# Kernel tuning notes

Measured on AMD Instinct MI355X. Metric: run time of the kernel, lower is better.

## Reference

```python
import jax, jax.numpy as jnp
import numpy as np

GAMMA = 1.0
BANDWIDTH = 0  # 0 => no Sakoe-Chiba band
LARGE = 1e30   # stand-in for +inf; exact in the softmin limit, NaN-safe under autodiff


def _pairwise_sq_dist(x, y):
    # x:[B,N,d], y:[B,M,d] -> D:[B,N,M] squared Euclidean
    x2 = jnp.sum(x * x, axis=-1)[:, :, None]
    y2 = jnp.sum(y * y, axis=-1)[:, None, :]
    return x2 + y2 - 2.0 * jnp.einsum('bnd,bmd->bnm', x, y)


def _softdtw(D, gamma=GAMMA, bw=BANDWIDTH):
    # Anti-diagonal wavefront: scan over p = i0 + j0 in [0, N+M-2].
    # Diagonal is stored indexed by row i0; carry = (diag p-2, diag p-1).
    B, N, M = D.shape
    idx = jnp.arange(N)

    def step(carry, p):
        prev2, prev = carry                      # each [B, N]
        j0 = p - idx                             # column index per row
        valid = (j0 >= 0) & (j0 < M)
        if bw > 0:
            valid = valid & (jnp.abs(idx - j0) <= bw)
        Dg = D[:, idx, jnp.clip(j0, 0, M - 1)]   # [B, N]
        inf_col = jnp.full((B, 1), LARGE, D.dtype)
        # R[i0-1, j0-1] lives on diag p-2 at row i0-1
        r_nw = jnp.concatenate([inf_col, prev2[:, :-1]], axis=1)
        # virtual boundary R[0,0] = 0 feeds cell (i0=0, j0=0)
        r_nw = jnp.where((idx == 0) & (p == 0), jnp.zeros((), D.dtype), r_nw)
        # R[i0-1, j0] on diag p-1 at row i0-1; R[i0, j0-1] on diag p-1 at row i0
        r_n = jnp.concatenate([inf_col, prev[:, :-1]], axis=1)
        r_w = prev
        # stable softmin with gamma smoothing
        r0, r1, r2 = -r_nw / gamma, -r_n / gamma, -r_w / gamma
        rmax = jnp.maximum(jnp.maximum(r0, r1), r2)
        rsum = jnp.exp(r0 - rmax) + jnp.exp(r1 - rmax) + jnp.exp(r2 - rmax)
        softmin = -gamma * (jnp.log(rsum) + rmax)
        cur = jnp.where(valid, Dg + softmin, LARGE)
        return (prev, cur), None

    init = (jnp.full((B, N), LARGE, D.dtype), jnp.full((B, N), LARGE, D.dtype))
    (_, last), _ = jax.lax.scan(step, init, jnp.arange(N + M - 1))
    # With bw == 0 (or bw >= |N-M|), the loss is R[:, N, M] == last diag at row N-1.
    return last[:, N - 1]


def setup_inputs() -> dict:
    key = jax.random.key(0)
    k1, k2 = jax.random.split(key)
    x = jax.random.normal(k1, (128, 512, 64), dtype=jnp.float32)
    y = jax.random.normal(k2, (128, 512, 64), dtype=jnp.float32)
    return {"x": x, "y": y}


def reference(x, y):
    D = _pairwise_sq_dist(x, y)
    return _softdtw(D)
```

## Files before the change

### kernel.cpp

```cpp
#include <hip/hip_runtime.h>
#include <hip/hip_bf16.h>

#define LARGE_F 1e30f
#define LOG2E_F 1.4426950408889634f
#define LN2_F   0.6931471805599453f

constexpr int BB = 128;
constexpr int NN = 512;
constexpr int MM = 512;
constexpr int KK = 64;
constexpr int PBATCH = 262656;
constexpr size_t NEED = (size_t)BB * PBATCH * 2 + 4096;

typedef __attribute__((ext_vector_type(8))) short short8;
typedef __attribute__((ext_vector_type(4))) float f32x4;

__device__ __forceinline__ float wave_shr1(float v, float bound) {
    const int r = __builtin_amdgcn_update_dpp(__float_as_int(bound), __float_as_int(v),
                                              0x138, 0xf, 0xf, false);
    return __int_as_float(r);
}

__device__ __forceinline__ unsigned pack_bf16(float a, float b) {
    __hip_bfloat16 ha = __float2bfloat16(a);
    __hip_bfloat16 hb = __float2bfloat16(b);
    return (unsigned)*(unsigned short*)&ha | ((unsigned)*(unsigned short*)&hb << 16);
}

__device__ __forceinline__ float fast_exp2(float x) { return __builtin_amdgcn_exp2f(x); }
__device__ __forceinline__ float fast_log2(float x) { return __builtin_amdgcn_logf(x); }

__global__ __launch_bounds__(256, 2) void sdtw_dist(const float* __restrict__ x,
                                                    const float* __restrict__ y,
                                                    unsigned short* __restrict__ Dws) {
    __shared__ __align__(16) unsigned short xbf[128][88];
    __shared__ __align__(16) unsigned short ybf[128][88];
    __shared__ float x2s[128], y2s[128];
    __shared__ float xpart[128][2], ypart[128][2];
    unsigned short (*dt)[132] = (unsigned short (*)[132])(&xbf[0][0]);

    const int bid  = blockIdx.x;
    const int xcd  = bid & 7, sidx = bid >> 3;
    const int g    = sidx >> 4, tile = sidx & 15;
    const int b    = xcd + (g << 3);
    const int ti   = (tile >> 2) << 7, tj = (tile & 3) << 7;
    const int t    = threadIdx.x;

    const float* xb = x + ((size_t)b * NN + ti) * KK;
    const float* yb = y + ((size_t)b * MM + tj) * KK;

    {
        const int r = t >> 1, h = t & 1;
        const float* xr = xb + r * KK + h * 32;
        const float* yr = yb + r * KK + h * 32;
        float sx = 0.f, sy = 0.f;
        unsigned xu[16], yu[16];
#pragma unroll
        for (int q = 0; q < 8; ++q) {
            const float4 v = *(const float4*)(xr + 4 * q);
            sx = fmaf(v.x, v.x, fmaf(v.y, v.y, fmaf(v.z, v.z, fmaf(v.w, v.w, sx))));
            xu[2 * q]     = pack_bf16(v.x, v.y);
            xu[2 * q + 1] = pack_bf16(v.z, v.w);
            const float4 u = *(const float4*)(yr + 4 * q);
            sy = fmaf(u.x, u.x, fmaf(u.y, u.y, fmaf(u.z, u.z, fmaf(u.w, u.w, sy))));
            yu[2 * q]     = pack_bf16(u.x, u.y);
            yu[2 * q + 1] = pack_bf16(u.z, u.w);
        }
#pragma unroll
        for (int q = 0; q < 4; ++q) {
            *(uint4*)(&xbf[r][h * 32 + q * 8]) = make_uint4(xu[4*q], xu[4*q+1], xu[4*q+2], xu[4*q+3]);
            *(uint4*)(&ybf[r][h * 32 + q * 8]) = make_uint4(yu[4*q], yu[4*q+1], yu[4*q+2], yu[4*q+3]);
        }
        xpart[r][h] = sx; ypart[r][h] = sy;
    }
    __syncthreads();
    if (t < 128) x2s[t] = xpart[t][0] + xpart[t][1];
    else         y2s[t - 128] = ypart[t - 128][0] + ypart[t - 128][1];
    __syncthreads();

    const int w    = t >> 6, lane = t & 63;
    const int wr   = (w >> 1) << 6, wc = (w & 1) << 6;
    const int fr   = lane & 15;
    const int fk   = (lane >> 4) << 3;

    f32x4 acc[4][4] = {};
#pragma unroll
    for (int c = 0; c < 2; ++c) {
        short8 A[4], Bf[4];
#pragma unroll
        for (int a = 0; a < 4; ++a)
            A[a] = *(const short8*)(&xbf[wr + (a << 4) + fr][(c << 5) + fk]);
#pragma unroll
        for (int bb = 0; bb < 4; ++bb)
            Bf[bb] = *(const short8*)(&ybf[wc + (bb << 4) + fr][(c << 5) + fk]);
#pragma unroll
        for (int a = 0; a < 4; ++a)
#pragma unroll
            for (int bb = 0; bb < 4; ++bb)
                acc[a][bb] = __builtin_amdgcn_mfma_f32_16x16x32_bf16(
                    A[a], Bf[bb], acc[a][bb], 0, 0, 0);
    }
    __syncthreads();

    {
        const int er = (lane >> 4) << 2;
        const int ec = lane & 15;
#pragma unroll
        for (int a = 0; a < 4; ++a) {
#pragma unroll
            for (int bb = 0; bb < 4; ++bb) {
                const int lcol = wc + (bb << 4) + ec;
                const float yy = y2s[lcol];
#pragma unroll
                for (int reg = 0; reg < 4; ++reg) {
                    const int lrow = wr + (a << 4) + er + reg;
                    const float d = (x2s[lrow] + yy - 2.f * acc[a][bb][reg]) * LOG2E_F;
                    __hip_bfloat16 hh = __float2bfloat16(d);
                    dt[lrow][lcol] = *(unsigned short*)&hh;
                }
            }
        }
    }
    __syncthreads();

    {
        unsigned short* Dg = Dws + (size_t)b * PBATCH;
#pragma unroll 4
        for (int r = w; r < 128; r += 4) {
            const int gi = ti + r;
            const int base = 512 * gi + (gi + tj);
            Dg[base + lane]      = dt[r][lane];
            Dg[base + lane + 64] = dt[r][lane + 64];
        }
    }
}

__global__ __launch_bounds__(512, 1) void sdtw_dp(const unsigned short* __restrict__ Dws,
                                                  float* __restrict__ out) {
    __shared__ __align__(16) float hnd[3][8][16];
    const int b    = blockIdx.x;
    const int tid  = threadIdx.x;
    const int lane = tid & 63;
    const int wv   = tid >> 6;
    const int k0   = wv << 2;

    if (tid < 384) ((float*)hnd)[tid] = LARGE_F;
    __syncthreads();

    const char* Dbase = (const char*)Dws;
    unsigned off = (unsigned)b * 525312u + (unsigned)tid * 1024u + (unsigned)(k0 << 5);

    float cur = LARGE_F;
    float nw  = (tid == 0) ? 0.f : LARGE_F;
    float res = 0.f;
    float hband_prev = LARGE_F;
    const bool haveup = (wv > 0);
    const bool l0     = (lane == 0);

    uint4 c0 = *(const uint4*)(Dbase + off);
    uint4 c1 = *(const uint4*)(Dbase + off + 16);
    off += 32;

    int m0 = 0, m1 = 2;
#pragma unroll 1
    for (int e = 0; e < 71; ++e) {
        const int k = e - wv;
        if (k >= k0 && k < k0 + 36) {
            const unsigned q[8] = {c0.x, c0.y, c0.z, c0.w, c1.x, c1.y, c1.z, c1.w};
            float d[16];
#pragma unroll
            for (int u = 0; u < 16; ++u) {
                const unsigned w_ = q[u >> 1];
                d[u] = __uint_as_float((u & 1) ? (w_ & 0xffff0000u) : (w_ << 16));
            }
            c0 = *(const uint4*)(Dbase + off);
            c1 = *(const uint4*)(Dbase + off + 16);
            off += 32;
            __builtin_amdgcn_sched_barrier(0);

            if (k == k0 && haveup) {
                const int m2 = 3 - m0 - m1;
                hband_prev = hnd[m2][wv - 1][15];
            }
            const float hband = haveup ? hnd[m1][wv - 1][lane & 15] : LARGE_F;
            float h[16];
#pragma unroll
            for (int u = 0; u < 16; ++u) {
                const float nvec = wave_shr1(cur, LARGE_F);
                const float hu = __int_as_float(__builtin_amdgcn_readlane(
                    __float_as_int((u == 0) ? hband_prev : hband),
                    (u == 0) ? 15 : (u - 1)));
                const float n  = (haveup && l0) ? hu : nvec;
                const float mn = fminf(fminf(cur, n), nw);
                const float mx = fmaxf(fmaxf(cur, n), nw);
                const float md = __builtin_amdgcn_fmed3f(cur, n, nw);
                const float sm = mn - fast_log2(1.f + fast_exp2(mn - md) + fast_exp2(mn - mx));
                const float newc = d[u] + sm;
                h[u] = newc;
                nw = n; cur = newc;
            }
            if (k == 63) res = h[14];
            hband_prev = hband;
            if (lane == 63) {
                *(float4*)(&hnd[m0][wv][0])  = make_float4(h[0], h[1], h[2], h[3]);
                *(float4*)(&hnd[m0][wv][4])  = make_float4(h[4], h[5], h[6], h[7]);
                *(float4*)(&hnd[m0][wv][8])  = make_float4(h[8], h[9], h[10], h[11]);
                *(float4*)(&hnd[m0][wv][12]) = make_float4(h[12], h[13], h[14], h[15]);
            }
        }
        asm volatile("s_waitcnt lgkmcnt(0)" ::: "memory");
        __builtin_amdgcn_s_barrier();
        m0 = (m0 == 2) ? 0 : m0 + 1;
        m1 = (m1 == 2) ? 0 : m1 + 1;
    }
    if (tid == 511) out[b] = res * LN2_F;
}

__global__ __launch_bounds__(512) void sdtw_fused_naive(const float* __restrict__ x,
                                                        const float* __restrict__ y,
                                                        float* __restrict__ out) {
    __shared__ float rbuf[3][NN];
    __shared__ float y2s[MM];
    const int b = blockIdx.x;
    const int i = threadIdx.x;

    const float* xrow  = x + ((size_t)b * NN + i) * KK;
    const float* ybase = y + (size_t)b * MM * KK;

    float xr[KK];
    float x2 = 0.f;
#pragma unroll
    for (int k = 0; k < KK; k += 4) {
        const float4 v = *(const float4*)(xrow + k);
        xr[k] = v.x; xr[k + 1] = v.y; xr[k + 2] = v.z; xr[k + 3] = v.w;
        x2 = fmaf(v.x, v.x, fmaf(v.y, v.y, fmaf(v.z, v.z, fmaf(v.w, v.w, x2))));
    }
    {
        const float* yrow = ybase + (size_t)i * KK;
        float s = 0.f;
#pragma unroll
        for (int k = 0; k < KK; k += 4) {
            const float4 v = *(const float4*)(yrow + k);
            s = fmaf(v.x, v.x, s); s = fmaf(v.y, v.y, s);
            s = fmaf(v.z, v.z, s); s = fmaf(v.w, v.w, s);
        }
        y2s[i] = s;
    }
    rbuf[0][i] = LARGE_F;
    rbuf[1][i] = LARGE_F;
    rbuf[2][i] = LARGE_F;

    float* row_w  = rbuf[0];
    float* row_p  = rbuf[2];
    float* row_p2 = rbuf[1];
    __syncthreads();

    float cur = LARGE_F;
    for (int p = 0; p < NN + MM - 1; ++p) {
        const int j0 = p - i;
        const bool valid = (j0 >= 0) && (j0 < MM);
        float dg = 0.f;
        if (valid) {
            const float* yrow = ybase + (size_t)j0 * KK;
            float dot = 0.f;
#pragma unroll
            for (int k = 0; k < KK; k += 4) {
                const float4 v = *(const float4*)(yrow + k);
                dot = fmaf(xr[k], v.x, dot);
                dot = fmaf(xr[k + 1], v.y, dot);
                dot = fmaf(xr[k + 2], v.z, dot);
                dot = fmaf(xr[k + 3], v.w, dot);
            }
            dg = x2 + y2s[j0] - 2.f * dot;
        }
        const float r_w  = row_p[i];
        const float r_n  = (i > 0) ? row_p[i - 1] : LARGE_F;
        const float r_nw = (i > 0) ? row_p2[i - 1] : ((p == 0) ? 0.f : LARGE_F);

        const float m = fminf(fminf(r_nw, r_n), r_w);
        const float s = __expf(m - r_nw) + __expf(m - r_n) + __expf(m - r_w);
        const float softmin = m - __logf(s);

        cur = valid ? (dg + softmin) : LARGE_F;
        row_w[i] = cur;
        __syncthreads();

        float* tmp = row_w;
        row_w = row_p2; row_p2 = row_p; row_p = tmp;
    }
    if (i == NN - 1) out[b] = cur;
}

extern "C" void kernel_launch(void* const* d_in, const int* in_sizes, int n_in,
                              void* d_out, int out_size, void* d_ws, size_t ws_size,
                              hipStream_t stream) {
    const float* x = (const float*)d_in[0];
    const float* y = (const float*)d_in[1];
    float* out = (float*)d_out;

    if (ws_size >= NEED) {
        unsigned short* Dws = (unsigned short*)d_ws;
        sdtw_dist<<<dim3(2048), 256, 0, stream>>>(x, y, Dws);
        sdtw_dp<<<dim3(BB), 512, 0, stream>>>(Dws, out);
    } else {
        sdtw_fused_naive<<<dim3(BB), 512, 0, stream>>>(x, y, out);
    }
}
```

Before: 107.5 us.

## Split soft-DTW DP into forward and backward half-triangles combined at anti-diagonal

Replaces the single full-wavefront DP per batch with two blocks per batch. One sweeps forward from the start and the other sweeps backward over a reversed view of the cost matrix, each covering only half of the anti-diagonals. A new combine kernel joins the two halves with a log-sum-exp over the meeting anti-diagonal. This halves the serial dependency chain and doubles the number of blocks to use more CUs. The price is an extra kernel launch, scalar strided bf16 loads on the backward path, and reliance on soft-DTW forward/backward decomposition being exact at the meeting cells.

New measurement: 110.3 us. +2.6%, slower.

```diff
diff --git a/kernel.cpp b/kernel.cpp
--- a/kernel.cpp
+++ b/kernel.cpp
@@ -10,7 +10,9 @@
 constexpr int MM = 512;
 constexpr int KK = 64;
 constexpr int PBATCH = 262656;
-constexpr size_t NEED = (size_t)BB * PBATCH * 2 + 4096;
+constexpr int EXPN   = 65536;
+constexpr size_t EXP_OFF = 67239936;
+constexpr size_t NEED = EXP_OFF + 4 * (size_t)EXPN * 4;
 
 typedef __attribute__((ext_vector_type(8))) short short8;
 typedef __attribute__((ext_vector_type(4))) float f32x4;
@@ -135,47 +137,68 @@
     }
 }
 
-__global__ __launch_bounds__(512, 1) void sdtw_dp(const unsigned short* __restrict__ Dws,
-                                                  float* __restrict__ out) {
+__global__ __launch_bounds__(512, 1) void sdtw_dp_tri(const unsigned short* __restrict__ Dws,
+                                                      float* __restrict__ exps) {
     __shared__ __align__(16) float hnd[3][8][16];
-    const int b    = blockIdx.x;
-    const int tid  = threadIdx.x;
-    const int lane = tid & 63;
-    const int wv   = tid >> 6;
-    const int k0   = wv << 2;
+    const int blk   = blockIdx.x;
+    const int batch = blk >> 1, dir = blk & 1;
+    const int tid   = threadIdx.x;
+    const int lane  = tid & 63;
+    const int wv    = tid >> 6;
+    const int k0    = wv << 2;
 
     if (tid < 384) ((float*)hnd)[tid] = LARGE_F;
     __syncthreads();
 
-    const char* Dbase = (const char*)Dws;
-    unsigned off = (unsigned)b * 525312u + (unsigned)tid * 1024u + (unsigned)(k0 << 5);
+    const unsigned short* Dp = Dws + (size_t)batch * PBATCH;
+    const char* Dbase = (const char*)Dp;
 
     float cur = LARGE_F;
     float nw  = (tid == 0) ? 0.f : LARGE_F;
-    float res = 0.f;
     float hband_prev = LARGE_F;
     const bool haveup = (wv > 0);
     const bool l0     = (lane == 0);
-
-    uint4 c0 = *(const uint4*)(Dbase + off);
-    uint4 c1 = *(const uint4*)(Dbase + off + 16);
-    off += 32;
+    float r510 = LARGE_F, r511 = LARGE_F;
+
+    unsigned off = (unsigned)tid * 1024u + ((unsigned)k0 << 5);
+    uint4 c0, c1;
+    unsigned short nb[16];
+    int base = 0;
+    if (dir == 0) {
+        c0 = *(const uint4*)(Dbase + off);
+        c1 = *(const uint4*)(Dbase + off + 16);
+        off += 32;
+    } else {
+        base = 512 * (511 - tid) + 1022 - (k0 << 4);
+#pragma unroll
+        for (int u = 0; u < 16; ++u) nb[u] = Dp[base - u];
+        base -= 16;
+    }
 
     int m0 = 0, m1 = 2;
 #pragma unroll 1
-    for (int e = 0; e < 71; ++e) {
+    for (int e = 0; e < 39; ++e) {
         const int k = e - wv;
-        if (k >= k0 && k < k0 + 36) {
-            const unsigned q[8] = {c0.x, c0.y, c0.z, c0.w, c1.x, c1.y, c1.z, c1.w};
+        if (k >= k0 && k <= 31) {
             float d[16];
-#pragma unroll
-            for (int u = 0; u < 16; ++u) {
-                const unsigned w_ = q[u >> 1];
-                d[u] = __uint_as_float((u & 1) ? (w_ & 0xffff0000u) : (w_ << 16));
-            }
-            c0 = *(const uint4*)(Dbase + off);
-            c1 = *(const uint4*)(Dbase + off + 16);
-            off += 32;
+            if (dir == 0) {
+                const unsigned q[8] = {c0.x, c0.y, c0.z, c0.w, c1.x, c1.y, c1.z, c1.w};
+#pragma unroll
+                for (int u = 0; u < 16; ++u) {
+                    const unsigned w_ = q[u >> 1];
+                    d[u] = __uint_as_float((u & 1) ? (w_ & 0xffff0000u) : (w_ << 16));
+                }
+                c0 = *(const uint4*)(Dbase + off);
+                c1 = *(const uint4*)(Dbase + off + 16);
+                off += 32;
+            } else {
+#pragma unroll
+                for (int u = 0; u < 16; ++u)
+                    d[u] = __uint_as_float((unsigned)nb[u] << 16);
+#pragma unroll
+                for (int u = 0; u < 16; ++u) nb[u] = Dp[base - u];
+                base -= 16;
+            }
             __builtin_amdgcn_sched_barrier(0);
 
             if (k == k0 && haveup) {
@@ -199,8 +222,8 @@
                 h[u] = newc;
                 nw = n; cur = newc;
             }
-            if (k == 63) res = h[14];
             hband_prev = hband;
+            if (k == 31) { r510 = h[14]; r511 = h[15]; }
             if (lane == 63) {
                 *(float4*)(&hnd[m0][wv][0])  = make_float4(h[0], h[1], h[2], h[3]);
                 *(float4*)(&hnd[m0][wv][4])  = make_float4(h[4], h[5], h[6], h[7]);
@@ -213,7 +236,48 @@
         m0 = (m0 == 2) ? 0 : m0 + 1;
         m1 = (m1 == 2) ? 0 : m1 + 1;
     }
-    if (tid == 511) out[b] = res * LN2_F;
+    exps[((dir << 1) + 0) * EXPN + (batch << 9) + tid] = r511;
+    exps[((dir << 1) + 1) * EXPN + (batch << 9) + tid] = r510;
+}
+
+__global__ __launch_bounds__(512) void sdtw_combine(const unsigned short* __restrict__ Dws,
+                                                    const float* __restrict__ exps,
+                                                    float* __restrict__ out) {
+    __shared__ float red[8];
+    const int b = blockIdx.x, i = threadIdx.x;
+    const int lane = i & 63, wv = i >> 6;
+
+    const float rf511 = exps[0 * EXPN + (b << 9) + i];
+    const float rf510 = exps[1 * EXPN + (b << 9) + i];
+    const float rb511 = exps[2 * EXPN + (b << 9) + (511 - i)];
+    const float rb510 = (i < 511) ? exps[3 * EXPN + (b << 9) + (510 - i)] : 0.f;
+    const unsigned short dsh = Dws[(size_t)b * PBATCH + (i << 9) + 511];
+    const float d511 = __uint_as_float((unsigned)dsh << 16);
+
+    const float t1 = d511 - rf511 - rb511;
+    const float t2 = (i < 511) ? (-rf510 - rb510) : -LARGE_F;
+
+    float m = fmaxf(t1, t2);
+#pragma unroll
+    for (int s_ = 1; s_ < 64; s_ <<= 1) m = fmaxf(m, __shfl_xor(m, s_));
+    if (lane == 0) red[wv] = m;
+    __syncthreads();
+    float M = red[0];
+#pragma unroll
+    for (int w_ = 1; w_ < 8; ++w_) M = fmaxf(M, red[w_]);
+    __syncthreads();
+
+    float s = fast_exp2(t1 - M) + ((i < 511) ? fast_exp2(t2 - M) : 0.f);
+#pragma unroll
+    for (int s_ = 1; s_ < 64; s_ <<= 1) s += __shfl_xor(s, s_);
+    if (lane == 0) red[wv] = s;
+    __syncthreads();
+    if (i == 0) {
+        float S = red[0];
+#pragma unroll
+        for (int w_ = 1; w_ < 8; ++w_) S += red[w_];
+        out[b] = -(M + fast_log2(S)) * LN2_F;
+    }
 }
 
 __global__ __launch_bounds__(512) void sdtw_fused_naive(const float* __restrict__ x,
@@ -300,8 +364,10 @@
 
     if (ws_size >= NEED) {
         unsigned short* Dws = (unsigned short*)d_ws;
+        float* exps = (float*)((char*)d_ws + EXP_OFF);
         sdtw_dist<<<dim3(2048), 256, 0, stream>>>(x, y, Dws);
-        sdtw_dp<<<dim3(BB), 512, 0, stream>>>(Dws, out);
+        sdtw_dp_tri<<<dim3(256), 512, 0, stream>>>(Dws, exps);
+        sdtw_combine<<<dim3(BB), 512, 0, stream>>>(Dws, exps, out);
     } else {
         sdtw_fused_naive<<<dim3(BB), 512, 0, stream>>>(x, y, out);
     }
```
